# Optimization experiments

Measured on AMD Instinct MI355X. Metric: run time of the kernel, lower is better.

Reference implementation:

```python
import jax, jax.numpy as jnp
import numpy as np

N, D, M, H, FF, L = 8192, 14, 36, 256, 2048, 2  # rows, d_model, material feats, mlp hidden, ffn, layers
EPS = 1e-5


def _ln(x, g, b):
    mu = jnp.mean(x, axis=-1, keepdims=True)
    var = jnp.mean((x - mu) ** 2, axis=-1, keepdims=True)
    return (x - mu) * jax.lax.rsqrt(var + EPS) * g + b


def setup_inputs() -> dict:
    key = jax.random.key(0)
    ks = iter(jax.random.split(key, 32))
    p = lambda shape, fan: jax.random.normal(next(ks), shape, jnp.float32) * (fan ** -0.5)
    return {
        "x": jax.random.normal(next(ks), (N, D), jnp.float32),
        "y": jax.random.normal(next(ks), (N, M), jnp.float32),
        # 2 post-LN TransformerEncoderLayers (nhead=1, dim_feedforward=2048, relu)
        "attn_wqkv": p((L, 3 * D, D), D), "attn_bqkv": p((L, 3 * D), D),
        "attn_wo": p((L, D, D), D), "attn_bo": p((L, D), D),
        "ln1_g": jnp.ones((L, D)), "ln1_b": jnp.zeros((L, D)),
        "ff_w1": p((L, FF, D), D), "ff_b1": p((L, FF), D),
        "ff_w2": p((L, D, FF), FF), "ff_b2": p((L, D), FF),
        "ln2_g": jnp.ones((L, D)), "ln2_b": jnp.zeros((L, D)),
        "fc1_w": p((D, D), D), "fc1_b": p((D,), D),
        "fc2_w": p((1, D), D), "fc2_b": p((1,), D),
        "fc3_w": p((H, D + M + 1), D + M + 1), "fc3_b": p((H,), D + M + 1),
        "fc4_w": p((H, H), H), "fc4_b": p((H,), H),
        "fc5_w": p((1, H), H), "fc5_b": p((1,), H),
    }


def reference(x, y, attn_wqkv, attn_bqkv, attn_wo, attn_bo, ln1_g, ln1_b,
              ff_w1, ff_b1, ff_w2, ff_b2, ln2_g, ln2_b,
              fc1_w, fc1_b, fc2_w, fc2_b, fc3_w, fc3_b, fc4_w, fc4_b, fc5_w, fc5_b):
    h = x  # [N, D]; batch of size 1 squeezed away
    for l in range(L):
        qkv = h @ attn_wqkv[l].T + attn_bqkv[l]            # [N, 3D]
        q, k, v = jnp.split(qkv, 3, axis=-1)
        scores = (q @ k.T) * (D ** -0.5)                   # [N, N]
        a = jax.nn.softmax(scores, axis=-1) @ v            # [N, D]
        a = a @ attn_wo[l].T + attn_bo[l]
        h = _ln(h + a, ln1_g[l], ln1_b[l])
        f = jax.nn.relu(h @ ff_w1[l].T + ff_b1[l]) @ ff_w2[l].T + ff_b2[l]
        h = _ln(h + f, ln2_g[l], ln2_b[l])
    x1 = h @ fc1_w.T + fc1_b                               # [N, D]
    size_out = (x1 @ fc2_w.T + fc2_b)[:, 0]                # [N]

    # batched replacement of the per-row python loop
    size_int = size_out.astype(jnp.int32)                  # trunc toward zero, like .int()
    size_f = size_int.astype(jnp.float32)[:, None]         # [N, 1]
    reg_in = jnp.concatenate([size_f, x, y], axis=1)       # [N, 1+D+M]
    r = jax.nn.relu(reg_in @ fc3_w.T + fc3_b)
    r = jax.nn.relu(r @ fc4_w.T + fc4_b)
    reg_values = (r @ fc5_w.T + fc5_b)[:, 0]               # [N]
    reg_values = jnp.where(size_int != 0, reg_values, 0.0)
    return size_out, reg_values
```

## Files before the change

### kernel.cpp

```cpp
#include <hip/hip_runtime.h>
#include <math.h>

#define NN 8192
#define DD 14
#define DP 16
#define FF 2048
#define HID 256
#define LN_EPS 1e-5f
#define QSCALE (1.4426950408889634f / 3.7416573867739413f)

typedef short bf16x8 __attribute__((ext_vector_type(8)));
typedef float f32x4 __attribute__((ext_vector_type(4)));

#define LOAD16(dst, srcp) { \
  const float4* _p = (const float4*)(srcp); \
  float4 _a = _p[0], _b = _p[1], _c = _p[2], _d = _p[3]; \
  dst[0]=_a.x; dst[1]=_a.y; dst[2]=_a.z; dst[3]=_a.w; \
  dst[4]=_b.x; dst[5]=_b.y; dst[6]=_b.z; dst[7]=_b.w; \
  dst[8]=_c.x; dst[9]=_c.y; dst[10]=_c.z; dst[11]=_c.w; \
  dst[12]=_d.x; dst[13]=_d.y; dst[14]=_d.z; dst[15]=_d.w; }

#define STORE16(dstp, src) { \
  float4* _p = (float4*)(dstp); \
  _p[0] = make_float4(src[0], src[1], src[2], src[3]); \
  _p[1] = make_float4(src[4], src[5], src[6], src[7]); \
  _p[2] = make_float4(src[8], src[9], src[10], src[11]); \
  _p[3] = make_float4(src[12], src[13], src[14], src[15]); }

static __device__ __forceinline__ float fast_exp2(float x) {
#if __has_builtin(__builtin_amdgcn_exp2f)
  return __builtin_amdgcn_exp2f(x);
#else
  return exp2f(x);
#endif
}

static __device__ __forceinline__ unsigned short bf_hi(float x) {
  return (unsigned short)(__float_as_uint(x) >> 16);
}
static __device__ __forceinline__ float bf_hi_f(float x) {
  return __uint_as_float(__float_as_uint(x) & 0xffff0000u);
}

static __device__ __forceinline__ void split8(const float* pv, bf16x8* ph, bf16x8* pl) {
  #pragma unroll
  for (int i = 0; i < 8; i++) {
    unsigned int u = __float_as_uint(pv[i]);
    (*ph)[i] = (short)(u >> 16);
    float rr = pv[i] - __uint_as_float(u & 0xffff0000u);
    (*pl)[i] = (short)(__float_as_uint(rr) >> 16);
  }
}

static __device__ __forceinline__ void qkv_compute_store(
    int r, const float* hr, const float* __restrict__ wqkv,
    const float* __restrict__ bqkv, unsigned int* __restrict__ Qpack,
    unsigned int* __restrict__ KB1, unsigned int* __restrict__ KB2,
    unsigned short* __restrict__ VhiT, unsigned short* __restrict__ VloT) {
  float q[14], k[14], v[14];
  #pragma unroll 6
  for (int c = 0; c < 42; c++) {
    const float* w = wqkv + c * 14;
    float s = bqkv[c];
    #pragma unroll
    for (int d = 0; d < 14; d++) s = fmaf(hr[d], w[d], s);
    if (c < 14)       q[c] = s * QSCALE;
    else if (c < 28)  k[c - 14] = s;
    else              v[c - 28] = s;
  }
  unsigned int qp[16], k1[16], k2[16];
  unsigned short qh[14], ql[14], kh[14], kl[14];
  #pragma unroll
  for (int d = 0; d < 14; d++) {
    qh[d] = bf_hi(q[d]);
    ql[d] = bf_hi(q[d] - bf_hi_f(q[d]));
    kh[d] = bf_hi(k[d]);
    kl[d] = bf_hi(k[d] - bf_hi_f(k[d]));
  }
  #pragma unroll
  for (int i = 0; i < 7; i++) {
    qp[i]     = (unsigned int)qh[2*i] | ((unsigned int)qh[2*i+1] << 16);
    qp[8 + i] = (unsigned int)ql[2*i] | ((unsigned int)ql[2*i+1] << 16);
    k1[i]     = (unsigned int)kh[2*i] | ((unsigned int)kh[2*i+1] << 16);
    k1[8 + i] = k1[i];
    k2[i]     = (unsigned int)kl[2*i] | ((unsigned int)kl[2*i+1] << 16);
    k2[8 + i] = k2[i];
  }
  qp[7] = 0; qp[15] = 0; k1[7] = 0; k1[15] = 0; k2[7] = 0; k2[15] = 0;
  uint4* Qp4 = (uint4*)(Qpack + (size_t)r * 16);
  uint4* K14 = (uint4*)(KB1 + (size_t)r * 16);
  uint4* K24 = (uint4*)(KB2 + (size_t)r * 16);
  #pragma unroll
  for (int i = 0; i < 4; i++) {
    Qp4[i] = make_uint4(qp[4*i], qp[4*i+1], qp[4*i+2], qp[4*i+3]);
    K14[i] = make_uint4(k1[4*i], k1[4*i+1], k1[4*i+2], k1[4*i+3]);
    K24[i] = make_uint4(k2[4*i], k2[4*i+1], k2[4*i+2], k2[4*i+3]);
  }
  #pragma unroll
  for (int d = 0; d < 14; d++) {
    VhiT[(size_t)d * NN + r] = bf_hi(v[d]);
    VloT[(size_t)d * NN + r] = bf_hi(v[d] - bf_hi_f(v[d]));
  }
  VhiT[(size_t)14 * NN + r] = 0x3F80;
  VhiT[(size_t)15 * NN + r] = 0;
  VloT[(size_t)14 * NN + r] = 0;
  VloT[(size_t)15 * NN + r] = 0;
}

static __device__ __forceinline__ void store_apack(unsigned int* dst, const float* o) {
  unsigned int qp[16];
  unsigned short hh[14], ll[14];
  #pragma unroll
  for (int d = 0; d < 14; d++) {
    hh[d] = bf_hi(o[d]);
    ll[d] = bf_hi(o[d] - bf_hi_f(o[d]));
  }
  #pragma unroll
  for (int i = 0; i < 7; i++) {
    qp[i]     = (unsigned int)hh[2*i] | ((unsigned int)hh[2*i+1] << 16);
    qp[8 + i] = (unsigned int)ll[2*i] | ((unsigned int)ll[2*i+1] << 16);
  }
  qp[7] = 0; qp[15] = 0;
  uint4* d4 = (uint4*)dst;
  #pragma unroll
  for (int i = 0; i < 4; i++)
    d4[i] = make_uint4(qp[4*i], qp[4*i+1], qp[4*i+2], qp[4*i+3]);
}

__global__ void pack_all(const float* __restrict__ w3, const float* __restrict__ w4,
                         const float* __restrict__ ffw1, const float* __restrict__ ffw2,
                         const float* __restrict__ x, const float* __restrict__ wqkv,
                         const float* __restrict__ bqkv, float* __restrict__ h,
                         unsigned int* __restrict__ Qpack,
                         unsigned int* __restrict__ KB1, unsigned int* __restrict__ KB2,
                         unsigned short* __restrict__ VhiT, unsigned short* __restrict__ VloT,
                         unsigned short* __restrict__ B3h, unsigned short* __restrict__ B3l,
                         unsigned short* __restrict__ B4h, unsigned short* __restrict__ B4l,
                         unsigned int* __restrict__ W1B1, unsigned int* __restrict__ W1B2,
                         unsigned short* __restrict__ W2h, unsigned short* __restrict__ W2l) {
  const int blk = blockIdx.x, tid = threadIdx.x;
  if (blk < 32) {
    int t = blk * 256 + tid;
    int lane = t & 63, ks = (t >> 6) & 7, nt = t >> 9;
    int n = nt * 16 + (lane & 15);
    int k0 = ks * 32 + (lane >> 4) * 8;
    unsigned int h4[4], l4[4];
    #pragma unroll
    for (int jj = 0; jj < 4; jj++) {
      unsigned short h2[2], l2[2];
      #pragma unroll
      for (int e = 0; e < 2; e++) {
        float v = w4[(size_t)n * 256 + k0 + jj * 2 + e];
        h2[e] = bf_hi(v);
        l2[e] = bf_hi(v - bf_hi_f(v));
      }
      h4[jj] = (unsigned int)h2[0] | ((unsigned int)h2[1] << 16);
      l4[jj] = (unsigned int)l2[0] | ((unsigned int)l2[1] << 16);
    }
    ((uint4*)B4h)[t] = make_uint4(h4[0], h4[1], h4[2], h4[3]);
    ((uint4*)B4l)[t] = make_uint4(l4[0], l4[1], l4[2], l4[3]);
    if (ks < 2) {
      int fi = (nt * 2 + ks) * 64 + lane;
      #pragma unroll
      for (int jj = 0; jj < 4; jj++) {
        unsigned short h2[2], l2[2];
        #pragma unroll
        for (int e = 0; e < 2; e++) {
          int k = k0 + jj * 2 + e;
          float v = (k < 51) ? w3[(size_t)n * 51 + k] : 0.f;
          h2[e] = bf_hi(v);
          l2[e] = bf_hi(v - bf_hi_f(v));
        }
        h4[jj] = (unsigned int)h2[0] | ((unsigned int)h2[1] << 16);
        l4[jj] = (unsigned int)l2[0] | ((unsigned int)l2[1] << 16);
      }
      ((uint4*)B3h)[fi] = make_uint4(h4[0], h4[1], h4[2], h4[3]);
      ((uint4*)B3l)[fi] = make_uint4(l4[0], l4[1], l4[2], l4[3]);
    }
  } else if (blk < 48) {
    int t = (blk - 32) * 256 + tid;
    int l = t >> 11, j = t & 2047;
    const float* wrow = ffw1 + ((size_t)l * FF + j) * 14;
    unsigned int k1[16], k2[16];
    unsigned short kh[14], kl[14];
    #pragma unroll
    for (int d = 0; d < 14; d++) {
      float v = wrow[d];
      kh[d] = bf_hi(v);
      kl[d] = bf_hi(v - bf_hi_f(v));
    }
    #pragma unroll
    for (int i = 0; i < 7; i++) {
      k1[i] = (unsigned int)kh[2*i] | ((unsigned int)kh[2*i+1] << 16);
      k1[8 + i] = k1[i];
      k2[i] = (unsigned int)kl[2*i] | ((unsigned int)kl[2*i+1] << 16);
      k2[8 + i] = k2[i];
    }
    k1[7] = 0; k1[15] = 0; k2[7] = 0; k2[15] = 0;
    uint4* d1 = (uint4*)(W1B1 + (size_t)t * 16);
    uint4* d2 = (uint4*)(W1B2 + (size_t)t * 16);
    #pragma unroll
    for (int i = 0; i < 4; i++) {
      d1[i] = make_uint4(k1[4*i], k1[4*i+1], k1[4*i+2], k1[4*i+3]);
      d2[i] = make_uint4(k2[4*i], k2[4*i+1], k2[4*i+2], k2[4*i+3]);
    }
  } else if (blk < 64) {
    int t = (blk - 48) * 256 + tid;
    int l = t >> 11, j = t & 2047;
    #pragma unroll
    for (int d = 0; d < 16; d++) {
      float v = (d < 14) ? ffw2[((size_t)l * 14 + d) * FF + j] : 0.f;
      W2h[((size_t)l * 16 + d) * FF + j] = bf_hi(v);
      W2l[((size_t)l * 16 + d) * FF + j] = bf_hi(v - bf_hi_f(v));
    }
  } else {
    int r = (blk - 64) * 256 + tid;
    float hr[16];
    #pragma unroll
    for (int d = 0; d < 14; d++) hr[d] = x[(size_t)r * 14 + d];
    hr[14] = 0.f; hr[15] = 0.f;
    STORE16(h + (size_t)r * DP, hr);
    qkv_compute_store(r, hr, wqkv, bqkv, Qpack, KB1, KB2, VhiT, VloT);
  }
}

__global__ __launch_bounds__(512, 2) void attn_flash(
    const unsigned int* __restrict__ Qpack, const unsigned int* __restrict__ KB1,
    const unsigned int* __restrict__ KB2, const unsigned short* __restrict__ VhiT,
    const unsigned short* __restrict__ VloT, float* __restrict__ h,
    const float* __restrict__ wo, const float* __restrict__ bo,
    const float* __restrict__ g, const float* __restrict__ b,
    unsigned int* __restrict__ Hpack) {
  __shared__ float Plds[8][32][36];
  __shared__ float sacc[8][32][16];
  const int tid = threadIdx.x;
  const int wave = tid >> 6;
  const int lane = tid & 63;
  const int lo4 = lane & 15;
  const int hi4 = lane >> 4;
  const int qbase = blockIdx.x * 32;

  const bf16x8* Qp = (const bf16x8*)Qpack;
  const bf16x8* B1 = (const bf16x8*)KB1;
  const bf16x8* B2 = (const bf16x8*)KB2;
  const bf16x8* Vh = (const bf16x8*)VhiT;
  const bf16x8* Vl = (const bf16x8*)VloT;

  bf16x8 aQ0 = Qp[(size_t)(qbase + lo4) * 4 + hi4];
  bf16x8 aQ1 = Qp[(size_t)(qbase + 16 + lo4) * 4 + hi4];
  f32x4 acc0 = {0.f, 0.f, 0.f, 0.f};
  f32x4 acc1 = {0.f, 0.f, 0.f, 0.f};
  const f32x4 zero = {0.f, 0.f, 0.f, 0.f};

  const int kstart = wave * 1024;
  for (int c = 0; c < 32; c++) {
    const int kb = kstart + c * 32;
    bf16x8 b1g0 = B1[(size_t)(kb + lo4) * 4 + hi4];
    bf16x8 b2g0 = B2[(size_t)(kb + lo4) * 4 + hi4];
    bf16x8 b1g1 = B1[(size_t)(kb + 16 + lo4) * 4 + hi4];
    bf16x8 b2g1 = B2[(size_t)(kb + 16 + lo4) * 4 + hi4];
    bf16x8 vh = Vh[(size_t)lo4 * 1024 + (kb >> 3) + hi4];
    bf16x8 vl = Vl[(size_t)lo4 * 1024 + (kb >> 3) + hi4];

    f32x4 s00 = __builtin_amdgcn_mfma_f32_16x16x32_bf16(aQ0, b1g0, zero, 0, 0, 0);
    f32x4 s01 = __builtin_amdgcn_mfma_f32_16x16x32_bf16(aQ0, b1g1, zero, 0, 0, 0);
    f32x4 s10 = __builtin_amdgcn_mfma_f32_16x16x32_bf16(aQ1, b1g0, zero, 0, 0, 0);
    f32x4 s11 = __builtin_amdgcn_mfma_f32_16x16x32_bf16(aQ1, b1g1, zero, 0, 0, 0);
    s00 = __builtin_amdgcn_mfma_f32_16x16x32_bf16(aQ0, b2g0, s00, 0, 0, 0);
    s01 = __builtin_amdgcn_mfma_f32_16x16x32_bf16(aQ0, b2g1, s01, 0, 0, 0);
    s10 = __builtin_amdgcn_mfma_f32_16x16x32_bf16(aQ1, b2g0, s10, 0, 0, 0);
    s11 = __builtin_amdgcn_mfma_f32_16x16x32_bf16(aQ1, b2g1, s11, 0, 0, 0);
    #pragma unroll
    for (int reg = 0; reg < 4; reg++) {
      Plds[wave][hi4 * 4 + reg][lo4]           = fast_exp2(s00[reg]);
      Plds[wave][hi4 * 4 + reg][16 + lo4]      = fast_exp2(s01[reg]);
      Plds[wave][16 + hi4 * 4 + reg][lo4]      = fast_exp2(s10[reg]);
      Plds[wave][16 + hi4 * 4 + reg][16 + lo4] = fast_exp2(s11[reg]);
    }
    __asm__ volatile("s_waitcnt lgkmcnt(0)" ::: "memory");
    const float4* p0 = (const float4*)&Plds[wave][lo4][hi4 * 8];
    const float4* p1 = (const float4*)&Plds[wave][16 + lo4][hi4 * 8];
    float4 a0 = p0[0], a1 = p0[1], c0 = p1[0], c1 = p1[1];
    float pv0[8] = {a0.x, a0.y, a0.z, a0.w, a1.x, a1.y, a1.z, a1.w};
    float pv1[8] = {c0.x, c0.y, c0.z, c0.w, c1.x, c1.y, c1.z, c1.w};
    bf16x8 ph0, pl0, ph1, pl1;
    split8(pv0, &ph0, &pl0);
    split8(pv1, &ph1, &pl1);
    acc0 = __builtin_amdgcn_mfma_f32_16x16x32_bf16(ph0, vh, acc0, 0, 0, 0);
    acc1 = __builtin_amdgcn_mfma_f32_16x16x32_bf16(ph1, vh, acc1, 0, 0, 0);
    acc0 = __builtin_amdgcn_mfma_f32_16x16x32_bf16(pl0, vh, acc0, 0, 0, 0);
    acc1 = __builtin_amdgcn_mfma_f32_16x16x32_bf16(pl1, vh, acc1, 0, 0, 0);
    acc0 = __builtin_amdgcn_mfma_f32_16x16x32_bf16(ph0, vl, acc0, 0, 0, 0);
    acc1 = __builtin_amdgcn_mfma_f32_16x16x32_bf16(ph1, vl, acc1, 0, 0, 0);
    __asm__ volatile("s_waitcnt lgkmcnt(0)" ::: "memory");
  }

  #pragma unroll
  for (int reg = 0; reg < 4; reg++) {
    sacc[wave][hi4 * 4 + reg][lo4] = acc0[reg];
    sacc[wave][16 + hi4 * 4 + reg][lo4] = acc1[reg];
  }
  __syncthreads();
  {
    int qq = tid >> 4, col = tid & 15;
    float v = 0.f;
    #pragma unroll
    for (int w = 0; w < 8; w++) v += sacc[w][qq][col];
    sacc[0][qq][col] = v;
  }
  __syncthreads();

  if (tid < 32) {
    int r = qbase + tid;
    float L = sacc[0][tid][14];
    float inv = 1.f / L;
    float a[14];
    #pragma unroll
    for (int d = 0; d < 14; d++) a[d] = sacc[0][tid][d] * inv;
    float hr[16];
    LOAD16(hr, h + (size_t)r * DP);
    float xx[14];
    #pragma unroll
    for (int i = 0; i < 14; i++) {
      float s = bo[i];
      #pragma unroll
      for (int d = 0; d < 14; d++) s = fmaf(wo[i * 14 + d], a[d], s);
      xx[i] = hr[i] + s;
    }
    float mu = 0.f;
    #pragma unroll
    for (int i = 0; i < 14; i++) mu += xx[i];
    mu *= (1.f / 14.f);
    float var = 0.f;
    #pragma unroll
    for (int i = 0; i < 14; i++) { float tt = xx[i] - mu; var = fmaf(tt, tt, var); }
    var *= (1.f / 14.f);
    float rs = rsqrtf(var + LN_EPS);
    float o[16];
    #pragma unroll
    for (int i = 0; i < 14; i++) o[i] = fmaf((xx[i] - mu) * rs, g[i], b[i]);
    o[14] = 0.f; o[15] = 0.f;
    STORE16(h + (size_t)r * DP, o);
    store_apack(Hpack + (size_t)r * 16, o);
  }
}

__global__ __launch_bounds__(512, 2) void ffn_flash_qkv(
    float* __restrict__ h, const unsigned int* __restrict__ Hpack,
    const unsigned int* __restrict__ W1B1, const unsigned int* __restrict__ W1B2,
    const unsigned short* __restrict__ W2h, const unsigned short* __restrict__ W2l,
    const float* __restrict__ b1, const float* __restrict__ b2,
    const float* __restrict__ g, const float* __restrict__ bb,
    const float* __restrict__ wqkv, const float* __restrict__ bqkv,
    unsigned int* __restrict__ Qpack, unsigned int* __restrict__ KB1,
    unsigned int* __restrict__ KB2, unsigned short* __restrict__ VhiT,
    unsigned short* __restrict__ VloT) {
  __shared__ float Plds[8][32][36];
  __shared__ float sacc[8][32][16];
  const int tid = threadIdx.x;
  const int wave = tid >> 6;
  const int lane = tid & 63;
  const int lo4 = lane & 15;
  const int hi4 = lane >> 4;
  const int qbase = blockIdx.x * 32;

  const bf16x8* Hp = (const bf16x8*)Hpack;
  const bf16x8* B1 = (const bf16x8*)W1B1;
  const bf16x8* B2 = (const bf16x8*)W1B2;
  const bf16x8* Vh = (const bf16x8*)W2h;
  const bf16x8* Vl = (const bf16x8*)W2l;

  bf16x8 aH0 = Hp[(size_t)(qbase + lo4) * 4 + hi4];
  bf16x8 aH1 = Hp[(size_t)(qbase + 16 + lo4) * 4 + hi4];
  f32x4 acc0 = {0.f, 0.f, 0.f, 0.f};
  f32x4 acc1 = {0.f, 0.f, 0.f, 0.f};
  const f32x4 zero = {0.f, 0.f, 0.f, 0.f};

  const int jstart = wave * 256;
  for (int c = 0; c < 8; c++) {
    const int jb = jstart + c * 32;
    bf16x8 b1g0 = B1[(size_t)(jb + lo4) * 4 + hi4];
    bf16x8 b2g0 = B2[(size_t)(jb + lo4) * 4 + hi4];
    bf16x8 b1g1 = B1[(size_t)(jb + 16 + lo4) * 4 + hi4];
    bf16x8 b2g1 = B2[(size_t)(jb + 16 + lo4) * 4 + hi4];
    bf16x8 vh = Vh[(size_t)lo4 * 256 + (jb >> 3) + hi4];
    bf16x8 vl = Vl[(size_t)lo4 * 256 + (jb >> 3) + hi4];
    float bb0 = b1[jb + lo4];
    float bb1 = b1[jb + 16 + lo4];

    f32x4 s00 = __builtin_amdgcn_mfma_f32_16x16x32_bf16(aH0, b1g0, zero, 0, 0, 0);
    f32x4 s01 = __builtin_amdgcn_mfma_f32_16x16x32_bf16(aH0, b1g1, zero, 0, 0, 0);
    f32x4 s10 = __builtin_amdgcn_mfma_f32_16x16x32_bf16(aH1, b1g0, zero, 0, 0, 0);
    f32x4 s11 = __builtin_amdgcn_mfma_f32_16x16x32_bf16(aH1, b1g1, zero, 0, 0, 0);
    s00 = __builtin_amdgcn_mfma_f32_16x16x32_bf16(aH0, b2g0, s00, 0, 0, 0);
    s01 = __builtin_amdgcn_mfma_f32_16x16x32_bf16(aH0, b2g1, s01, 0, 0, 0);
    s10 = __builtin_amdgcn_mfma_f32_16x16x32_bf16(aH1, b2g0, s10, 0, 0, 0);
    s11 = __builtin_amdgcn_mfma_f32_16x16x32_bf16(aH1, b2g1, s11, 0, 0, 0);
    #pragma unroll
    for (int reg = 0; reg < 4; reg++) {
      Plds[wave][hi4 * 4 + reg][lo4]           = fmaxf(s00[reg] + bb0, 0.f);
      Plds[wave][hi4 * 4 + reg][16 + lo4]      = fmaxf(s01[reg] + bb1, 0.f);
      Plds[wave][16 + hi4 * 4 + reg][lo4]      = fmaxf(s10[reg] + bb0, 0.f);
      Plds[wave][16 + hi4 * 4 + reg][16 + lo4] = fmaxf(s11[reg] + bb1, 0.f);
    }
    __asm__ volatile("s_waitcnt lgkmcnt(0)" ::: "memory");
    const float4* p0 = (const float4*)&Plds[wave][lo4][hi4 * 8];
    const float4* p1 = (const float4*)&Plds[wave][16 + lo4][hi4 * 8];
    float4 a0 = p0[0], a1 = p0[1], c0 = p1[0], c1 = p1[1];
    float pv0[8] = {a0.x, a0.y, a0.z, a0.w, a1.x, a1.y, a1.z, a1.w};
    float pv1[8] = {c0.x, c0.y, c0.z, c0.w, c1.x, c1.y, c1.z, c1.w};
    bf16x8 th0, tl0, th1, tl1;
    split8(pv0, &th0, &tl0);
    split8(pv1, &th1, &tl1);
    acc0 = __builtin_amdgcn_mfma_f32_16x16x32_bf16(th0, vh, acc0, 0, 0, 0);
    acc1 = __builtin_amdgcn_mfma_f32_16x16x32_bf16(th1, vh, acc1, 0, 0, 0);
    acc0 = __builtin_amdgcn_mfma_f32_16x16x32_bf16(tl0, vh, acc0, 0, 0, 0);
    acc1 = __builtin_amdgcn_mfma_f32_16x16x32_bf16(tl1, vh, acc1, 0, 0, 0);
    acc0 = __builtin_amdgcn_mfma_f32_16x16x32_bf16(th0, vl, acc0, 0, 0, 0);
    acc1 = __builtin_amdgcn_mfma_f32_16x16x32_bf16(th1, vl, acc1, 0, 0, 0);
    __asm__ volatile("s_waitcnt lgkmcnt(0)" ::: "memory");
  }

  #pragma unroll
  for (int reg = 0; reg < 4; reg++) {
    sacc[wave][hi4 * 4 + reg][lo4] = acc0[reg];
    sacc[wave][16 + hi4 * 4 + reg][lo4] = acc1[reg];
  }
  __syncthreads();
  {
    int qq = tid >> 4, col = tid & 15;
    float v = 0.f;
    #pragma unroll
    for (int w = 0; w < 8; w++) v += sacc[w][qq][col];
    sacc[0][qq][col] = v;
  }
  __syncthreads();

  if (tid < 32) {
    int r = qbase + tid;
    float hr[16];
    LOAD16(hr, h + (size_t)r * DP);
    float xx[14];
    #pragma unroll
    for (int i = 0; i < 14; i++) xx[i] = hr[i] + sacc[0][tid][i] + b2[i];
    float mu = 0.f;
    #pragma unroll
    for (int i = 0; i < 14; i++) mu += xx[i];
    mu *= (1.f / 14.f);
    float var = 0.f;
    #pragma unroll
    for (int i = 0; i < 14; i++) { float tt = xx[i] - mu; var = fmaf(tt, tt, var); }
    var *= (1.f / 14.f);
    float rs = rsqrtf(var + LN_EPS);
    float o[16];
    #pragma unroll
    for (int i = 0; i < 14; i++) o[i] = fmaf((xx[i] - mu) * rs, g[i], bb[i]);
    o[14] = 0.f; o[15] = 0.f;
    STORE16(h + (size_t)r * DP, o);
    qkv_compute_store(r, o, wqkv, bqkv, Qpack, KB1, KB2, VhiT, VloT);
  }
}

__global__ __launch_bounds__(256, 4) void ffn_tail(
    const float* __restrict__ h, const unsigned int* __restrict__ Hpack,
    const unsigned int* __restrict__ W1B1, const unsigned int* __restrict__ W1B2,
    const unsigned short* __restrict__ W2h, const unsigned short* __restrict__ W2l,
    const float* __restrict__ b1,
    const float* __restrict__ b2, const float* __restrict__ g, const float* __restrict__ b,
    const float* __restrict__ fc1w, const float* __restrict__ fc1b,
    const float* __restrict__ fc2w, const float* __restrict__ fc2b,
    const float* __restrict__ x, const float* __restrict__ y,
    const unsigned short* __restrict__ B3h, const unsigned short* __restrict__ B3l,
    const float* __restrict__ b3,
    const unsigned short* __restrict__ B4h, const unsigned short* __restrict__ B4l,
    const float* __restrict__ b4,
    const float* __restrict__ w5, const float* __restrict__ b5,
    float* __restrict__ out, float* __restrict__ outr) {
  __shared__ float PldsT[4][16][36];
  __shared__ float saccT[4][16][16];
  __shared__ alignas(16) unsigned short Ah[16][72], Al[16][72];
  __shared__ alignas(16) unsigned short R1h[16][264], R1l[16][264];
  __shared__ float sred[4][16][16];
  __shared__ float szf[16];
  const int tid = threadIdx.x;
  const int wave = tid >> 6;
  const int lane = tid & 63;
  const int lo4 = lane & 15;
  const int hi4 = lane >> 4;
  const int rbase = blockIdx.x * 16;
  const f32x4 zero = {0.f, 0.f, 0.f, 0.f};

  {
    const bf16x8* Hp = (const bf16x8*)Hpack;
    const bf16x8* B1 = (const bf16x8*)W1B1;
    const bf16x8* B2 = (const bf16x8*)W1B2;
    const bf16x8* Vh = (const bf16x8*)W2h;
    const bf16x8* Vl = (const bf16x8*)W2l;
    bf16x8 aH0 = Hp[(size_t)(rbase + lo4) * 4 + hi4];
    f32x4 acc0 = zero;
    const int jstart = wave * 512;
    for (int c = 0; c < 16; c++) {
      const int jb = jstart + c * 32;
      bf16x8 b1g0 = B1[(size_t)(jb + lo4) * 4 + hi4];
      bf16x8 b2g0 = B2[(size_t)(jb + lo4) * 4 + hi4];
      bf16x8 b1g1 = B1[(size_t)(jb + 16 + lo4) * 4 + hi4];
      bf16x8 b2g1 = B2[(size_t)(jb + 16 + lo4) * 4 + hi4];
      bf16x8 vh = Vh[(size_t)lo4 * 256 + (jb >> 3) + hi4];
      bf16x8 vl = Vl[(size_t)lo4 * 256 + (jb >> 3) + hi4];
      float bb0 = b1[jb + lo4];
      float bb1 = b1[jb + 16 + lo4];

      f32x4 s00 = __builtin_amdgcn_mfma_f32_16x16x32_bf16(aH0, b1g0, zero, 0, 0, 0);
      f32x4 s01 = __builtin_amdgcn_mfma_f32_16x16x32_bf16(aH0, b1g1, zero, 0, 0, 0);
      s00 = __builtin_amdgcn_mfma_f32_16x16x32_bf16(aH0, b2g0, s00, 0, 0, 0);
      s01 = __builtin_amdgcn_mfma_f32_16x16x32_bf16(aH0, b2g1, s01, 0, 0, 0);
      #pragma unroll
      for (int reg = 0; reg < 4; reg++) {
        PldsT[wave][hi4 * 4 + reg][lo4]      = fmaxf(s00[reg] + bb0, 0.f);
        PldsT[wave][hi4 * 4 + reg][16 + lo4] = fmaxf(s01[reg] + bb1, 0.f);
      }
      __asm__ volatile("s_waitcnt lgkmcnt(0)" ::: "memory");
      const float4* p0 = (const float4*)&PldsT[wave][lo4][hi4 * 8];
      float4 a0 = p0[0], a1 = p0[1];
      float pv0[8] = {a0.x, a0.y, a0.z, a0.w, a1.x, a1.y, a1.z, a1.w};
      bf16x8 th0, tl0;
      split8(pv0, &th0, &tl0);
      acc0 = __builtin_amdgcn_mfma_f32_16x16x32_bf16(th0, vh, acc0, 0, 0, 0);
      acc0 = __builtin_amdgcn_mfma_f32_16x16x32_bf16(tl0, vh, acc0, 0, 0, 0);
      acc0 = __builtin_amdgcn_mfma_f32_16x16x32_bf16(th0, vl, acc0, 0, 0, 0);
      __asm__ volatile("s_waitcnt lgkmcnt(0)" ::: "memory");
    }
    #pragma unroll
    for (int reg = 0; reg < 4; reg++)
      saccT[wave][hi4 * 4 + reg][lo4] = acc0[reg];
  }
  __syncthreads();
  {
    int qq = tid >> 4, col = tid & 15;
    float v = saccT[0][qq][col] + saccT[1][qq][col] + saccT[2][qq][col] + saccT[3][qq][col];
    saccT[0][qq][col] = v;
  }
  __syncthreads();

  if (tid < 16) {
    int r = rbase + tid;
    float hr[16];
    LOAD16(hr, h + (size_t)r * DP);
    float xx[14];
    #pragma unroll
    for (int i = 0; i < 14; i++) xx[i] = hr[i] + saccT[0][tid][i] + b2[i];
    float mu = 0.f;
    #pragma unroll
    for (int i = 0; i < 14; i++) mu += xx[i];
    mu *= (1.f / 14.f);
    float var = 0.f;
    #pragma unroll
    for (int i = 0; i < 14; i++) { float tt = xx[i] - mu; var = fmaf(tt, tt, var); }
    var *= (1.f / 14.f);
    float rs = rsqrtf(var + LN_EPS);
    float o[14];
    #pragma unroll
    for (int i = 0; i < 14; i++) o[i] = fmaf((xx[i] - mu) * rs, g[i], b[i]);
    float s = fc2b[0];
    #pragma unroll
    for (int i = 0; i < 14; i++) {
      float tt = fc1b[i];
      #pragma unroll
      for (int d = 0; d < 14; d++) tt = fmaf(fc1w[i * 14 + d], o[d], tt);
      s = fmaf(tt, fc2w[i], s);
    }
    out[r] = s;
    int si = (int)s;
    szf[tid] = (float)si;
  }
  __syncthreads();

  for (int idx = tid; idx < 16 * 64; idx += 256) {
    int m = idx >> 6, k = idx & 63;
    int r = rbase + m;
    float v = 0.f;
    if (k == 0)       v = szf[m];
    else if (k < 15)  v = x[(size_t)r * 14 + (k - 1)];
    else if (k < 51)  v = y[(size_t)r * 36 + (k - 15)];
    Ah[m][k] = bf_hi(v);
    Al[m][k] = bf_hi(v - bf_hi_f(v));
  }
  __syncthreads();

  f32x4 acc[4];
  #pragma unroll
  for (int nt = 0; nt < 4; nt++) acc[nt] = zero;
  #pragma unroll
  for (int ks = 0; ks < 2; ks++) {
    bf16x8 ah = *(const bf16x8*)&Ah[lo4][ks * 32 + hi4 * 8];
    bf16x8 al = *(const bf16x8*)&Al[lo4][ks * 32 + hi4 * 8];
    #pragma unroll
    for (int nt = 0; nt < 4; nt++) {
      int fi = ((wave * 4 + nt) * 2 + ks) * 64 + lane;
      bf16x8 bh = ((const bf16x8*)B3h)[fi];
      bf16x8 bl = ((const bf16x8*)B3l)[fi];
      acc[nt] = __builtin_amdgcn_mfma_f32_16x16x32_bf16(ah, bh, acc[nt], 0, 0, 0);
      acc[nt] = __builtin_amdgcn_mfma_f32_16x16x32_bf16(al, bh, acc[nt], 0, 0, 0);
      acc[nt] = __builtin_amdgcn_mfma_f32_16x16x32_bf16(ah, bl, acc[nt], 0, 0, 0);
    }
  }
  #pragma unroll
  for (int nt = 0; nt < 4; nt++) {
    int n = (wave * 4 + nt) * 16 + lo4;
    float bbv = b3[n];
    #pragma unroll
    for (int reg = 0; reg < 4; reg++) {
      int m = hi4 * 4 + reg;
      float v = fmaxf(acc[nt][reg] + bbv, 0.f);
      R1h[m][n] = bf_hi(v);
      R1l[m][n] = bf_hi(v - bf_hi_f(v));
    }
  }
  __syncthreads();

  #pragma unroll
  for (int nt = 0; nt < 4; nt++) acc[nt] = zero;
  #pragma unroll
  for (int ks = 0; ks < 8; ks++) {
    bf16x8 ah = *(const bf16x8*)&R1h[lo4][ks * 32 + hi4 * 8];
    bf16x8 al = *(const bf16x8*)&R1l[lo4][ks * 32 + hi4 * 8];
    #pragma unroll
    for (int nt = 0; nt < 4; nt++) {
      int fi = ((wave * 4 + nt) * 8 + ks) * 64 + lane;
      bf16x8 bh = ((const bf16x8*)B4h)[fi];
      bf16x8 bl = ((const bf16x8*)B4l)[fi];
      acc[nt] = __builtin_amdgcn_mfma_f32_16x16x32_bf16(ah, bh, acc[nt], 0, 0, 0);
      acc[nt] = __builtin_amdgcn_mfma_f32_16x16x32_bf16(al, bh, acc[nt], 0, 0, 0);
      acc[nt] = __builtin_amdgcn_mfma_f32_16x16x32_bf16(ah, bl, acc[nt], 0, 0, 0);
    }
  }
  float s4[4] = {0.f, 0.f, 0.f, 0.f};
  #pragma unroll
  for (int nt = 0; nt < 4; nt++) {
    int n = (wave * 4 + nt) * 16 + lo4;
    float bbv = b4[n], ww = w5[n];
    #pragma unroll
    for (int reg = 0; reg < 4; reg++)
      s4[reg] = fmaf(fmaxf(acc[nt][reg] + bbv, 0.f), ww, s4[reg]);
  }
  #pragma unroll
  for (int reg = 0; reg < 4; reg++) sred[wave][hi4 * 4 + reg][lo4] = s4[reg];
  __syncthreads();

  if (tid < 16) {
    float t = b5[0];
    #pragma unroll
    for (int w = 0; w < 4; w++) {
      const float4* p = (const float4*)&sred[w][tid][0];
      float4 a0 = p[0], a1 = p[1], a2 = p[2], a3 = p[3];
      t += ((a0.x + a0.y) + (a0.z + a0.w)) + ((a1.x + a1.y) + (a1.z + a1.w)) +
           ((a2.x + a2.y) + (a2.z + a2.w)) + ((a3.x + a3.y) + (a3.z + a3.w));
    }
    float sz = szf[tid];
    outr[rbase + tid] = (sz != 0.f) ? t : 0.f;
  }
}

extern "C" void kernel_launch(void* const* d_in, const int* in_sizes, int n_in,
                              void* d_out, int out_size, void* d_ws, size_t ws_size,
                              hipStream_t stream) {
  const float* x    = (const float*)d_in[0];
  const float* y    = (const float*)d_in[1];
  const float* wqkv = (const float*)d_in[2];
  const float* bqkv = (const float*)d_in[3];
  const float* wo   = (const float*)d_in[4];
  const float* bo   = (const float*)d_in[5];
  const float* ln1g = (const float*)d_in[6];
  const float* ln1b = (const float*)d_in[7];
  const float* ffw1 = (const float*)d_in[8];
  const float* ffb1 = (const float*)d_in[9];
  const float* ffw2 = (const float*)d_in[10];
  const float* ffb2 = (const float*)d_in[11];
  const float* ln2g = (const float*)d_in[12];
  const float* ln2b = (const float*)d_in[13];
  const float* fc1w = (const float*)d_in[14];
  const float* fc1b = (const float*)d_in[15];
  const float* fc2w = (const float*)d_in[16];
  const float* fc2b = (const float*)d_in[17];
  const float* fc3w = (const float*)d_in[18];
  const float* fc3b = (const float*)d_in[19];
  const float* fc4w = (const float*)d_in[20];
  const float* fc4b = (const float*)d_in[21];
  const float* fc5w = (const float*)d_in[22];
  const float* fc5b = (const float*)d_in[23];

  float* ws = (float*)d_ws;
  float*          h     = ws;
  unsigned int*   Qpack = (unsigned int*)(ws + 131072);
  unsigned int*   KB1   = (unsigned int*)(ws + 262144);
  unsigned int*   KB2   = (unsigned int*)(ws + 393216);
  unsigned short* VhiT  = (unsigned short*)(ws + 524288);
  unsigned short* VloT  = (unsigned short*)(ws + 589824);
  unsigned int*   Hpack = (unsigned int*)(ws + 655360);
  unsigned short* B3h   = (unsigned short*)(ws + 2891776);
  unsigned short* B3l   = (unsigned short*)(ws + 2899968);
  unsigned short* B4h   = (unsigned short*)(ws + 2908160);
  unsigned short* B4l   = (unsigned short*)(ws + 2940928);
  unsigned int*   W1B1  = (unsigned int*)(ws + 2973696);
  unsigned int*   W1B2  = (unsigned int*)(ws + 3039232);
  unsigned short* W2h   = (unsigned short*)(ws + 3104768);
  unsigned short* W2l   = (unsigned short*)(ws + 3137536);

  float* out = (float*)d_out;

  pack_all<<<96, 256, 0, stream>>>(fc3w, fc4w, ffw1, ffw2, x, wqkv, bqkv, h,
                                   Qpack, KB1, KB2, VhiT, VloT,
                                   B3h, B3l, B4h, B4l, W1B1, W1B2, W2h, W2l);

  attn_flash<<<256, 512, 0, stream>>>(Qpack, KB1, KB2, VhiT, VloT, h,
                                      wo, bo, ln1g, ln1b, Hpack);
  ffn_flash_qkv<<<256, 512, 0, stream>>>(h, Hpack, W1B1, W1B2, W2h, W2l,
                                         ffb1, ffb2, ln2g, ln2b,
                                         wqkv + 42 * 14, bqkv + 42,
                                         Qpack, KB1, KB2, VhiT, VloT);
  attn_flash<<<256, 512, 0, stream>>>(Qpack, KB1, KB2, VhiT, VloT, h,
                                      wo + 196, bo + 14, ln1g + 14, ln1b + 14, Hpack);
  ffn_tail<<<512, 256, 0, stream>>>(h, Hpack,
                                    W1B1 + (size_t)2048 * 16, W1B2 + (size_t)2048 * 16,
                                    W2h + (size_t)16 * FF, W2l + (size_t)16 * FF,
                                    ffb1 + FF, ffb2 + 14, ln2g + 14, ln2b + 14,
                                    fc1w, fc1b, fc2w, fc2b, x, y,
                                    B3h, B3l, fc3b, B4h, B4l, fc4b,
                                    fc5w, fc5b, out, out + NN);
}
```

Baseline: 244.9 us.

## Fuse attention with FFN per layer and software-pipeline the P·V stage

Merges each layer's attention and FFN kernels into one kernel, so five launches become three and the intermediate h/Hpack round trip through global memory goes away. Layer-1 QKV now goes into separate double buffers, so the fused layer-0 kernel never overwrites inputs that other blocks are still reading. Both the attention and FFN inner loops are software-pipelined: the LDS read and P·V MFMA for chunk c-1 are issued after the score MFMAs for chunk c, which drops the explicit lgkmcnt waits. The tail MLP now handles 32 rows per 512-thread block. The costs are more shared memory, higher register pressure, and an occupancy hint of 4 blocks per CU that may not be reachable.

```diff
diff --git a/kernel.cpp b/kernel.cpp
--- a/kernel.cpp
+++ b/kernel.cpp
@@ -125,6 +125,37 @@
   #pragma unroll
   for (int i = 0; i < 4; i++)
     d4[i] = make_uint4(qp[4*i], qp[4*i+1], qp[4*i+2], qp[4*i+3]);
+}
+
+static __device__ __forceinline__ void combine_ln1(
+    const float* srow, const float* hr, const float* __restrict__ wo,
+    const float* __restrict__ bo, const float* __restrict__ g,
+    const float* __restrict__ b, float* o) {
+  float L = srow[14];
+  float inv = 1.f / L;
+  float a[14];
+  #pragma unroll
+  for (int d = 0; d < 14; d++) a[d] = srow[d] * inv;
+  float xx[14];
+  #pragma unroll
+  for (int i = 0; i < 14; i++) {
+    float s = bo[i];
+    #pragma unroll
+    for (int d = 0; d < 14; d++) s = fmaf(wo[i * 14 + d], a[d], s);
+    xx[i] = hr[i] + s;
+  }
+  float mu = 0.f;
+  #pragma unroll
+  for (int i = 0; i < 14; i++) mu += xx[i];
+  mu *= (1.f / 14.f);
+  float var = 0.f;
+  #pragma unroll
+  for (int i = 0; i < 14; i++) { float tt = xx[i] - mu; var = fmaf(tt, tt, var); }
+  var *= (1.f / 14.f);
+  float rs = rsqrtf(var + LN_EPS);
+  #pragma unroll
+  for (int i = 0; i < 14; i++) o[i] = fmaf((xx[i] - mu) * rs, g[i], b[i]);
+  o[14] = 0.f; o[15] = 0.f;
 }
 
 __global__ void pack_all(const float* __restrict__ w3, const float* __restrict__ w4,
@@ -224,37 +255,26 @@
   }
 }
 
-__global__ __launch_bounds__(512, 2) void attn_flash(
-    const unsigned int* __restrict__ Qpack, const unsigned int* __restrict__ KB1,
-    const unsigned int* __restrict__ KB2, const unsigned short* __restrict__ VhiT,
-    const unsigned short* __restrict__ VloT, float* __restrict__ h,
-    const float* __restrict__ wo, const float* __restrict__ bo,
-    const float* __restrict__ g, const float* __restrict__ b,
-    unsigned int* __restrict__ Hpack) {
-  __shared__ float Plds[8][32][36];
-  __shared__ float sacc[8][32][16];
-  const int tid = threadIdx.x;
-  const int wave = tid >> 6;
-  const int lane = tid & 63;
-  const int lo4 = lane & 15;
-  const int hi4 = lane >> 4;
-  const int qbase = blockIdx.x * 32;
-
-  const bf16x8* Qp = (const bf16x8*)Qpack;
-  const bf16x8* B1 = (const bf16x8*)KB1;
-  const bf16x8* B2 = (const bf16x8*)KB2;
-  const bf16x8* Vh = (const bf16x8*)VhiT;
-  const bf16x8* Vl = (const bf16x8*)VloT;
-
+static __device__ __forceinline__ void attn_core(
+    const bf16x8* __restrict__ Qp, const bf16x8* __restrict__ B1,
+    const bf16x8* __restrict__ B2, const bf16x8* __restrict__ Vh,
+    const bf16x8* __restrict__ Vl, int qbase, int wave, int lo4, int hi4,
+    float (*Pl)[36], f32x4* o0, f32x4* o1) {
+  const f32x4 zero = {0.f, 0.f, 0.f, 0.f};
   bf16x8 aQ0 = Qp[(size_t)(qbase + lo4) * 4 + hi4];
   bf16x8 aQ1 = Qp[(size_t)(qbase + 16 + lo4) * 4 + hi4];
-  f32x4 acc0 = {0.f, 0.f, 0.f, 0.f};
-  f32x4 acc1 = {0.f, 0.f, 0.f, 0.f};
-  const f32x4 zero = {0.f, 0.f, 0.f, 0.f};
-
+  f32x4 acc0 = zero, acc1 = zero;
   const int kstart = wave * 1024;
+  float4 ra0, ra1, rc0, rc1;
+  const float4* p0 = (const float4*)&Pl[lo4][hi4 * 8];
+  const float4* p1 = (const float4*)&Pl[16 + lo4][hi4 * 8];
+
   for (int c = 0; c < 32; c++) {
     const int kb = kstart + c * 32;
+    if (c > 0) {
+      ra0 = p0[0]; ra1 = p0[1]; rc0 = p1[0]; rc1 = p1[1];
+      __asm__ volatile("" ::: "memory");
+    }
     bf16x8 b1g0 = B1[(size_t)(kb + lo4) * 4 + hi4];
     bf16x8 b2g0 = B2[(size_t)(kb + lo4) * 4 + hi4];
     bf16x8 b1g1 = B1[(size_t)(kb + 16 + lo4) * 4 + hi4];
@@ -272,119 +292,69 @@
     s11 = __builtin_amdgcn_mfma_f32_16x16x32_bf16(aQ1, b2g1, s11, 0, 0, 0);
     #pragma unroll
     for (int reg = 0; reg < 4; reg++) {
-      Plds[wave][hi4 * 4 + reg][lo4]           = fast_exp2(s00[reg]);
-      Plds[wave][hi4 * 4 + reg][16 + lo4]      = fast_exp2(s01[reg]);
-      Plds[wave][16 + hi4 * 4 + reg][lo4]      = fast_exp2(s10[reg]);
-      Plds[wave][16 + hi4 * 4 + reg][16 + lo4] = fast_exp2(s11[reg]);
-    }
-    __asm__ volatile("s_waitcnt lgkmcnt(0)" ::: "memory");
-    const float4* p0 = (const float4*)&Plds[wave][lo4][hi4 * 8];
-    const float4* p1 = (const float4*)&Plds[wave][16 + lo4][hi4 * 8];
+      Pl[hi4 * 4 + reg][lo4]           = fast_exp2(s00[reg]);
+      Pl[hi4 * 4 + reg][16 + lo4]      = fast_exp2(s01[reg]);
+      Pl[16 + hi4 * 4 + reg][lo4]      = fast_exp2(s10[reg]);
+      Pl[16 + hi4 * 4 + reg][16 + lo4] = fast_exp2(s11[reg]);
+    }
+    if (c > 0) {
+      const int kbp = kb - 32;
+      bf16x8 vhp = Vh[(size_t)lo4 * 1024 + (kbp >> 3) + hi4];
+      bf16x8 vlp = Vl[(size_t)lo4 * 1024 + (kbp >> 3) + hi4];
+      float pv0[8] = {ra0.x, ra0.y, ra0.z, ra0.w, ra1.x, ra1.y, ra1.z, ra1.w};
+      float pv1[8] = {rc0.x, rc0.y, rc0.z, rc0.w, rc1.x, rc1.y, rc1.z, rc1.w};
+      bf16x8 ph0, pl0, ph1, pl1;
+      split8(pv0, &ph0, &pl0);
+      split8(pv1, &ph1, &pl1);
+      acc0 = __builtin_amdgcn_mfma_f32_16x16x32_bf16(ph0, vhp, acc0, 0, 0, 0);
+      acc1 = __builtin_amdgcn_mfma_f32_16x16x32_bf16(ph1, vhp, acc1, 0, 0, 0);
+      acc0 = __builtin_amdgcn_mfma_f32_16x16x32_bf16(pl0, vhp, acc0, 0, 0, 0);
+      acc1 = __builtin_amdgcn_mfma_f32_16x16x32_bf16(pl1, vhp, acc1, 0, 0, 0);
+      acc0 = __builtin_amdgcn_mfma_f32_16x16x32_bf16(ph0, vlp, acc0, 0, 0, 0);
+      acc1 = __builtin_amdgcn_mfma_f32_16x16x32_bf16(ph1, vlp, acc1, 0, 0, 0);
+    }
+  }
+  {
+    const int kbp = kstart + 31 * 32;
+    bf16x8 vhp = Vh[(size_t)lo4 * 1024 + (kbp >> 3) + hi4];
+    bf16x8 vlp = Vl[(size_t)lo4 * 1024 + (kbp >> 3) + hi4];
     float4 a0 = p0[0], a1 = p0[1], c0 = p1[0], c1 = p1[1];
     float pv0[8] = {a0.x, a0.y, a0.z, a0.w, a1.x, a1.y, a1.z, a1.w};
     float pv1[8] = {c0.x, c0.y, c0.z, c0.w, c1.x, c1.y, c1.z, c1.w};
     bf16x8 ph0, pl0, ph1, pl1;
     split8(pv0, &ph0, &pl0);
     split8(pv1, &ph1, &pl1);
-    acc0 = __builtin_amdgcn_mfma_f32_16x16x32_bf16(ph0, vh, acc0, 0, 0, 0);
-    acc1 = __builtin_amdgcn_mfma_f32_16x16x32_bf16(ph1, vh, acc1, 0, 0, 0);
-    acc0 = __builtin_amdgcn_mfma_f32_16x16x32_bf16(pl0, vh, acc0, 0, 0, 0);
-    acc1 = __builtin_amdgcn_mfma_f32_16x16x32_bf16(pl1, vh, acc1, 0, 0, 0);
-    acc0 = __builtin_amdgcn_mfma_f32_16x16x32_bf16(ph0, vl, acc0, 0, 0, 0);
-    acc1 = __builtin_amdgcn_mfma_f32_16x16x32_bf16(ph1, vl, acc1, 0, 0, 0);
-    __asm__ volatile("s_waitcnt lgkmcnt(0)" ::: "memory");
-  }
-
-  #pragma unroll
-  for (int reg = 0; reg < 4; reg++) {
-    sacc[wave][hi4 * 4 + reg][lo4] = acc0[reg];
-    sacc[wave][16 + hi4 * 4 + reg][lo4] = acc1[reg];
-  }
-  __syncthreads();
-  {
-    int qq = tid >> 4, col = tid & 15;
-    float v = 0.f;
-    #pragma unroll
-    for (int w = 0; w < 8; w++) v += sacc[w][qq][col];
-    sacc[0][qq][col] = v;
-  }
-  __syncthreads();
-
-  if (tid < 32) {
-    int r = qbase + tid;
-    float L = sacc[0][tid][14];
-    float inv = 1.f / L;
-    float a[14];
-    #pragma unroll
-    for (int d = 0; d < 14; d++) a[d] = sacc[0][tid][d] * inv;
-    float hr[16];
-    LOAD16(hr, h + (size_t)r * DP);
-    float xx[14];
-    #pragma unroll
-    for (int i = 0; i < 14; i++) {
-      float s = bo[i];
-      #pragma unroll
-      for (int d = 0; d < 14; d++) s = fmaf(wo[i * 14 + d], a[d], s);
-      xx[i] = hr[i] + s;
-    }
-    float mu = 0.f;
-    #pragma unroll
-    for (int i = 0; i < 14; i++) mu += xx[i];
-    mu *= (1.f / 14.f);
-    float var = 0.f;
-    #pragma unroll
-    for (int i = 0; i < 14; i++) { float tt = xx[i] - mu; var = fmaf(tt, tt, var); }
-    var *= (1.f / 14.f);
-    float rs = rsqrtf(var + LN_EPS);
-    float o[16];
-    #pragma unroll
-    for (int i = 0; i < 14; i++) o[i] = fmaf((xx[i] - mu) * rs, g[i], b[i]);
-    o[14] = 0.f; o[15] = 0.f;
-    STORE16(h + (size_t)r * DP, o);
-    store_apack(Hpack + (size_t)r * 16, o);
-  }
-}
-
-__global__ __launch_bounds__(512, 2) void ffn_flash_qkv(
-    float* __restrict__ h, const unsigned int* __restrict__ Hpack,
-    const unsigned int* __restrict__ W1B1, const unsigned int* __restrict__ W1B2,
-    const unsigned short* __restrict__ W2h, const unsigned short* __restrict__ W2l,
-    const float* __restrict__ b1, const float* __restrict__ b2,
-    const float* __restrict__ g, const float* __restrict__ bb,
-    const float* __restrict__ wqkv, const float* __restrict__ bqkv,
-    unsigned int* __restrict__ Qpack, unsigned int* __restrict__ KB1,
-    unsigned int* __restrict__ KB2, unsigned short* __restrict__ VhiT,
-    unsigned short* __restrict__ VloT) {
-  __shared__ float Plds[8][32][36];
-  __shared__ float sacc[8][32][16];
-  const int tid = threadIdx.x;
-  const int wave = tid >> 6;
-  const int lane = tid & 63;
-  const int lo4 = lane & 15;
-  const int hi4 = lane >> 4;
-  const int qbase = blockIdx.x * 32;
-
-  const bf16x8* Hp = (const bf16x8*)Hpack;
-  const bf16x8* B1 = (const bf16x8*)W1B1;
-  const bf16x8* B2 = (const bf16x8*)W1B2;
-  const bf16x8* Vh = (const bf16x8*)W2h;
-  const bf16x8* Vl = (const bf16x8*)W2l;
-
-  bf16x8 aH0 = Hp[(size_t)(qbase + lo4) * 4 + hi4];
-  bf16x8 aH1 = Hp[(size_t)(qbase + 16 + lo4) * 4 + hi4];
-  f32x4 acc0 = {0.f, 0.f, 0.f, 0.f};
-  f32x4 acc1 = {0.f, 0.f, 0.f, 0.f};
+    acc0 = __builtin_amdgcn_mfma_f32_16x16x32_bf16(ph0, vhp, acc0, 0, 0, 0);
+    acc1 = __builtin_amdgcn_mfma_f32_16x16x32_bf16(ph1, vhp, acc1, 0, 0, 0);
+    acc0 = __builtin_amdgcn_mfma_f32_16x16x32_bf16(pl0, vhp, acc0, 0, 0, 0);
+    acc1 = __builtin_amdgcn_mfma_f32_16x16x32_bf16(pl1, vhp, acc1, 0, 0, 0);
+    acc0 = __builtin_amdgcn_mfma_f32_16x16x32_bf16(ph0, vlp, acc0, 0, 0, 0);
+    acc1 = __builtin_amdgcn_mfma_f32_16x16x32_bf16(ph1, vlp, acc1, 0, 0, 0);
+  }
+  *o0 = acc0; *o1 = acc1;
+}
+
+static __device__ __forceinline__ void ffn_core(
+    bf16x8 aH0, bf16x8 aH1, const bf16x8* __restrict__ B1,
+    const bf16x8* __restrict__ B2, const bf16x8* __restrict__ Vh,
+    const bf16x8* __restrict__ Vl, const float* __restrict__ b1,
+    int jstart, int lo4, int hi4, float (*Pl)[36], f32x4* o0, f32x4* o1) {
   const f32x4 zero = {0.f, 0.f, 0.f, 0.f};
-
-  const int jstart = wave * 256;
+  f32x4 acc0 = zero, acc1 = zero;
+  float4 ra0, ra1, rc0, rc1;
+  const float4* p0 = (const float4*)&Pl[lo4][hi4 * 8];
+  const float4* p1 = (const float4*)&Pl[16 + lo4][hi4 * 8];
+
   for (int c = 0; c < 8; c++) {
     const int jb = jstart + c * 32;
+    if (c > 0) {
+      ra0 = p0[0]; ra1 = p0[1]; rc0 = p1[0]; rc1 = p1[1];
+      __asm__ volatile("" ::: "memory");
+    }
     bf16x8 b1g0 = B1[(size_t)(jb + lo4) * 4 + hi4];
     bf16x8 b2g0 = B2[(size_t)(jb + lo4) * 4 + hi4];
     bf16x8 b1g1 = B1[(size_t)(jb + 16 + lo4) * 4 + hi4];
     bf16x8 b2g1 = B2[(size_t)(jb + 16 + lo4) * 4 + hi4];
-    bf16x8 vh = Vh[(size_t)lo4 * 256 + (jb >> 3) + hi4];
-    bf16x8 vl = Vl[(size_t)lo4 * 256 + (jb >> 3) + hi4];
     float bb0 = b1[jb + lo4];
     float bb1 = b1[jb + 16 + lo4];
 
@@ -398,33 +368,85 @@
     s11 = __builtin_amdgcn_mfma_f32_16x16x32_bf16(aH1, b2g1, s11, 0, 0, 0);
     #pragma unroll
     for (int reg = 0; reg < 4; reg++) {
-      Plds[wave][hi4 * 4 + reg][lo4]           = fmaxf(s00[reg] + bb0, 0.f);
-      Plds[wave][hi4 * 4 + reg][16 + lo4]      = fmaxf(s01[reg] + bb1, 0.f);
-      Plds[wave][16 + hi4 * 4 + reg][lo4]      = fmaxf(s10[reg] + bb0, 0.f);
-      Plds[wave][16 + hi4 * 4 + reg][16 + lo4] = fmaxf(s11[reg] + bb1, 0.f);
-    }
-    __asm__ volatile("s_waitcnt lgkmcnt(0)" ::: "memory");
-    const float4* p0 = (const float4*)&Plds[wave][lo4][hi4 * 8];
-    const float4* p1 = (const float4*)&Plds[wave][16 + lo4][hi4 * 8];
+      Pl[hi4 * 4 + reg][lo4]           = fmaxf(s00[reg] + bb0, 0.f);
+      Pl[hi4 * 4 + reg][16 + lo4]      = fmaxf(s01[reg] + bb1, 0.f);
+      Pl[16 + hi4 * 4 + reg][lo4]      = fmaxf(s10[reg] + bb0, 0.f);
+      Pl[16 + hi4 * 4 + reg][16 + lo4] = fmaxf(s11[reg] + bb1, 0.f);
+    }
+    if (c > 0) {
+      const int jbp = jb - 32;
+      bf16x8 vhp = Vh[(size_t)lo4 * 256 + (jbp >> 3) + hi4];
+      bf16x8 vlp = Vl[(size_t)lo4 * 256 + (jbp >> 3) + hi4];
+      float pv0[8] = {ra0.x, ra0.y, ra0.z, ra0.w, ra1.x, ra1.y, ra1.z, ra1.w};
+      float pv1[8] = {rc0.x, rc0.y, rc0.z, rc0.w, rc1.x, rc1.y, rc1.z, rc1.w};
+      bf16x8 th0, tl0, th1, tl1;
+      split8(pv0, &th0, &tl0);
+      split8(pv1, &th1, &tl1);
+      acc0 = __builtin_amdgcn_mfma_f32_16x16x32_bf16(th0, vhp, acc0, 0, 0, 0);
+      acc1 = __builtin_amdgcn_mfma_f32_16x16x32_bf16(th1, vhp, acc1, 0, 0, 0);
+      acc0 = __builtin_amdgcn_mfma_f32_16x16x32_bf16(tl0, vhp, acc0, 0, 0, 0);
+      acc1 = __builtin_amdgcn_mfma_f32_16x16x32_bf16(tl1, vhp, acc1, 0, 0, 0);
+      acc0 = __builtin_amdgcn_mfma_f32_16x16x32_bf16(th0, vlp, acc0, 0, 0, 0);
+      acc1 = __builtin_amdgcn_mfma_f32_16x16x32_bf16(th1, vlp, acc1, 0, 0, 0);
+    }
+  }
+  {
+    const int jbp = jstart + 7 * 32;
+    bf16x8 vhp = Vh[(size_t)lo4 * 256 + (jbp >> 3) + hi4];
+    bf16x8 vlp = Vl[(size_t)lo4 * 256 + (jbp >> 3) + hi4];
     float4 a0 = p0[0], a1 = p0[1], c0 = p1[0], c1 = p1[1];
     float pv0[8] = {a0.x, a0.y, a0.z, a0.w, a1.x, a1.y, a1.z, a1.w};
     float pv1[8] = {c0.x, c0.y, c0.z, c0.w, c1.x, c1.y, c1.z, c1.w};
     bf16x8 th0, tl0, th1, tl1;
     split8(pv0, &th0, &tl0);
     split8(pv1, &th1, &tl1);
-    acc0 = __builtin_amdgcn_mfma_f32_16x16x32_bf16(th0, vh, acc0, 0, 0, 0);
-    acc1 = __builtin_amdgcn_mfma_f32_16x16x32_bf16(th1, vh, acc1, 0, 0, 0);
-    acc0 = __builtin_amdgcn_mfma_f32_16x16x32_bf16(tl0, vh, acc0, 0, 0, 0);
-    acc1 = __builtin_amdgcn_mfma_f32_16x16x32_bf16(tl1, vh, acc1, 0, 0, 0);
-    acc0 = __builtin_amdgcn_mfma_f32_16x16x32_bf16(th0, vl, acc0, 0, 0, 0);
-    acc1 = __builtin_amdgcn_mfma_f32_16x16x32_bf16(th1, vl, acc1, 0, 0, 0);
-    __asm__ volatile("s_waitcnt lgkmcnt(0)" ::: "memory");
-  }
-
+    acc0 = __builtin_amdgcn_mfma_f32_16x16x32_bf16(th0, vhp, acc0, 0, 0, 0);
+    acc1 = __builtin_amdgcn_mfma_f32_16x16x32_bf16(th1, vhp, acc1, 0, 0, 0);
+    acc0 = __builtin_amdgcn_mfma_f32_16x16x32_bf16(tl0, vhp, acc0, 0, 0, 0);
+    acc1 = __builtin_amdgcn_mfma_f32_16x16x32_bf16(tl1, vhp, acc1, 0, 0, 0);
+    acc0 = __builtin_amdgcn_mfma_f32_16x16x32_bf16(th0, vlp, acc0, 0, 0, 0);
+    acc1 = __builtin_amdgcn_mfma_f32_16x16x32_bf16(th1, vlp, acc1, 0, 0, 0);
+  }
+  *o0 = acc0; *o1 = acc1;
+}
+
+#define SMEM_BYTES 57472
+
+__global__ __launch_bounds__(512, 4) void layer0_fused(
+    const unsigned int* __restrict__ Qpack, const unsigned int* __restrict__ KB1,
+    const unsigned int* __restrict__ KB2, const unsigned short* __restrict__ VhiT,
+    const unsigned short* __restrict__ VloT, float* __restrict__ h,
+    const float* __restrict__ wo, const float* __restrict__ bo,
+    const float* __restrict__ g1, const float* __restrict__ b1n,
+    const unsigned int* __restrict__ W1B1, const unsigned int* __restrict__ W1B2,
+    const unsigned short* __restrict__ W2h, const unsigned short* __restrict__ W2l,
+    const float* __restrict__ fb1, const float* __restrict__ fb2,
+    const float* __restrict__ g2, const float* __restrict__ b2n,
+    const float* __restrict__ wqkv1, const float* __restrict__ bqkv1,
+    unsigned int* __restrict__ Qpack1, unsigned int* __restrict__ KB1_1,
+    unsigned int* __restrict__ KB2_1, unsigned short* __restrict__ VhiT1,
+    unsigned short* __restrict__ VloT1) {
+  __shared__ alignas(16) char smem[SMEM_BYTES];
+  const int tid = threadIdx.x;
+  const int wave = tid >> 6;
+  const int lane = tid & 63;
+  const int lo4 = lane & 15;
+  const int hi4 = lane >> 4;
+  const int qbase = blockIdx.x * 32;
+
+  float (*Pl)[36] = (float(*)[36])(smem + wave * 4608);
+  float (*sacc)[32][16] = (float(*)[32][16])(smem + 36864);
+  float (*hrow)[16] = (float(*)[16])(smem + 53248);
+  unsigned int (*Hl)[16] = (unsigned int(*)[16])(smem + 55296);
+
+  f32x4 a0, a1;
+  attn_core((const bf16x8*)Qpack, (const bf16x8*)KB1, (const bf16x8*)KB2,
+            (const bf16x8*)VhiT, (const bf16x8*)VloT, qbase, wave, lo4, hi4,
+            Pl, &a0, &a1);
   #pragma unroll
   for (int reg = 0; reg < 4; reg++) {
-    sacc[wave][hi4 * 4 + reg][lo4] = acc0[reg];
-    sacc[wave][16 + hi4 * 4 + reg][lo4] = acc1[reg];
+    sacc[wave][hi4 * 4 + reg][lo4] = a0[reg];
+    sacc[wave][16 + hi4 * 4 + reg][lo4] = a1[reg];
   }
   __syncthreads();
   {
@@ -435,14 +457,44 @@
     sacc[0][qq][col] = v;
   }
   __syncthreads();
-
   if (tid < 32) {
     int r = qbase + tid;
     float hr[16];
     LOAD16(hr, h + (size_t)r * DP);
+    float o[16];
+    combine_ln1(&sacc[0][tid][0], hr, wo, bo, g1, b1n, o);
+    #pragma unroll
+    for (int i = 0; i < 16; i++) hrow[tid][i] = o[i];
+    store_apack(&Hl[tid][0], o);
+  }
+  __syncthreads();
+
+  bf16x8 aH0 = *(const bf16x8*)&Hl[lo4][hi4 * 4];
+  bf16x8 aH1 = *(const bf16x8*)&Hl[16 + lo4][hi4 * 4];
+  f32x4 f0, f1;
+  ffn_core(aH0, aH1, (const bf16x8*)W1B1, (const bf16x8*)W1B2,
+           (const bf16x8*)W2h, (const bf16x8*)W2l, fb1, wave * 256,
+           lo4, hi4, Pl, &f0, &f1);
+  __syncthreads();
+  #pragma unroll
+  for (int reg = 0; reg < 4; reg++) {
+    sacc[wave][hi4 * 4 + reg][lo4] = f0[reg];
+    sacc[wave][16 + hi4 * 4 + reg][lo4] = f1[reg];
+  }
+  __syncthreads();
+  {
+    int qq = tid >> 4, col = tid & 15;
+    float v = 0.f;
+    #pragma unroll
+    for (int w = 0; w < 8; w++) v += sacc[w][qq][col];
+    sacc[0][qq][col] = v;
+  }
+  __syncthreads();
+  if (tid < 32) {
+    int r = qbase + tid;
     float xx[14];
     #pragma unroll
-    for (int i = 0; i < 14; i++) xx[i] = hr[i] + sacc[0][tid][i] + b2[i];
+    for (int i = 0; i < 14; i++) xx[i] = hrow[tid][i] + sacc[0][tid][i] + fb2[i];
     float mu = 0.f;
     #pragma unroll
     for (int i = 0; i < 14; i++) mu += xx[i];
@@ -454,19 +506,23 @@
     float rs = rsqrtf(var + LN_EPS);
     float o[16];
     #pragma unroll
-    for (int i = 0; i < 14; i++) o[i] = fmaf((xx[i] - mu) * rs, g[i], bb[i]);
+    for (int i = 0; i < 14; i++) o[i] = fmaf((xx[i] - mu) * rs, g2[i], b2n[i]);
     o[14] = 0.f; o[15] = 0.f;
     STORE16(h + (size_t)r * DP, o);
-    qkv_compute_store(r, o, wqkv, bqkv, Qpack, KB1, KB2, VhiT, VloT);
-  }
-}
-
-__global__ __launch_bounds__(256, 4) void ffn_tail(
-    const float* __restrict__ h, const unsigned int* __restrict__ Hpack,
+    qkv_compute_store(r, o, wqkv1, bqkv1, Qpack1, KB1_1, KB2_1, VhiT1, VloT1);
+  }
+}
+
+__global__ __launch_bounds__(512, 4) void layer1_tail(
+    const unsigned int* __restrict__ Qpack, const unsigned int* __restrict__ KB1,
+    const unsigned int* __restrict__ KB2, const unsigned short* __restrict__ VhiT,
+    const unsigned short* __restrict__ VloT, const float* __restrict__ h,
+    const float* __restrict__ wo, const float* __restrict__ bo,
+    const float* __restrict__ g1, const float* __restrict__ b1n,
     const unsigned int* __restrict__ W1B1, const unsigned int* __restrict__ W1B2,
     const unsigned short* __restrict__ W2h, const unsigned short* __restrict__ W2l,
-    const float* __restrict__ b1,
-    const float* __restrict__ b2, const float* __restrict__ g, const float* __restrict__ b,
+    const float* __restrict__ fb1, const float* __restrict__ fb2,
+    const float* __restrict__ g2, const float* __restrict__ b2n,
     const float* __restrict__ fc1w, const float* __restrict__ fc1b,
     const float* __restrict__ fc2w, const float* __restrict__ fc2b,
     const float* __restrict__ x, const float* __restrict__ y,
@@ -476,79 +532,77 @@
     const float* __restrict__ b4,
     const float* __restrict__ w5, const float* __restrict__ b5,
     float* __restrict__ out, float* __restrict__ outr) {
-  __shared__ float PldsT[4][16][36];
-  __shared__ float saccT[4][16][16];
-  __shared__ alignas(16) unsigned short Ah[16][72], Al[16][72];
-  __shared__ alignas(16) unsigned short R1h[16][264], R1l[16][264];
-  __shared__ float sred[4][16][16];
-  __shared__ float szf[16];
+  __shared__ alignas(16) char smem[SMEM_BYTES];
   const int tid = threadIdx.x;
   const int wave = tid >> 6;
   const int lane = tid & 63;
   const int lo4 = lane & 15;
   const int hi4 = lane >> 4;
-  const int rbase = blockIdx.x * 16;
+  const int qbase = blockIdx.x * 32;
   const f32x4 zero = {0.f, 0.f, 0.f, 0.f};
 
-  {
-    const bf16x8* Hp = (const bf16x8*)Hpack;
-    const bf16x8* B1 = (const bf16x8*)W1B1;
-    const bf16x8* B2 = (const bf16x8*)W1B2;
-    const bf16x8* Vh = (const bf16x8*)W2h;
-    const bf16x8* Vl = (const bf16x8*)W2l;
-    bf16x8 aH0 = Hp[(size_t)(rbase + lo4) * 4 + hi4];
-    f32x4 acc0 = zero;
-    const int jstart = wave * 512;
-    for (int c = 0; c < 16; c++) {
-      const int jb = jstart + c * 32;
-      bf16x8 b1g0 = B1[(size_t)(jb + lo4) * 4 + hi4];
-      bf16x8 b2g0 = B2[(size_t)(jb + lo4) * 4 + hi4];
-      bf16x8 b1g1 = B1[(size_t)(jb + 16 + lo4) * 4 + hi4];
-      bf16x8 b2g1 = B2[(size_t)(jb + 16 + lo4) * 4 + hi4];
-      bf16x8 vh = Vh[(size_t)lo4 * 256 + (jb >> 3) + hi4];
-      bf16x8 vl = Vl[(size_t)lo4 * 256 + (jb >> 3) + hi4];
-      float bb0 = b1[jb + lo4];
-      float bb1 = b1[jb + 16 + lo4];
-
-      f32x4 s00 = __builtin_amdgcn_mfma_f32_16x16x32_bf16(aH0, b1g0, zero, 0, 0, 0);
-      f32x4 s01 = __builtin_amdgcn_mfma_f32_16x16x32_bf16(aH0, b1g1, zero, 0, 0, 0);
-      s00 = __builtin_amdgcn_mfma_f32_16x16x32_bf16(aH0, b2g0, s00, 0, 0, 0);
-      s01 = __builtin_amdgcn_mfma_f32_16x16x32_bf16(aH0, b2g1, s01, 0, 0, 0);
-      #pragma unroll
-      for (int reg = 0; reg < 4; reg++) {
-        PldsT[wave][hi4 * 4 + reg][lo4]      = fmaxf(s00[reg] + bb0, 0.f);
-        PldsT[wave][hi4 * 4 + reg][16 + lo4] = fmaxf(s01[reg] + bb1, 0.f);
-      }
-      __asm__ volatile("s_waitcnt lgkmcnt(0)" ::: "memory");
-      const float4* p0 = (const float4*)&PldsT[wave][lo4][hi4 * 8];
-      float4 a0 = p0[0], a1 = p0[1];
-      float pv0[8] = {a0.x, a0.y, a0.z, a0.w, a1.x, a1.y, a1.z, a1.w};
-      bf16x8 th0, tl0;
-      split8(pv0, &th0, &tl0);
-      acc0 = __builtin_amdgcn_mfma_f32_16x16x32_bf16(th0, vh, acc0, 0, 0, 0);
-      acc0 = __builtin_amdgcn_mfma_f32_16x16x32_bf16(tl0, vh, acc0, 0, 0, 0);
-      acc0 = __builtin_amdgcn_mfma_f32_16x16x32_bf16(th0, vl, acc0, 0, 0, 0);
-      __asm__ volatile("s_waitcnt lgkmcnt(0)" ::: "memory");
-    }
-    #pragma unroll
-    for (int reg = 0; reg < 4; reg++)
-      saccT[wave][hi4 * 4 + reg][lo4] = acc0[reg];
+  float (*Pl)[36] = (float(*)[36])(smem + wave * 4608);
+  float (*sacc)[32][16] = (float(*)[32][16])(smem + 36864);
+  float (*hrow)[16] = (float(*)[16])(smem + 53248);
+  unsigned int (*Hl)[16] = (unsigned int(*)[16])(smem + 55296);
+  float* szf = (float*)(smem + 57344);
+
+  f32x4 a0, a1;
+  attn_core((const bf16x8*)Qpack, (const bf16x8*)KB1, (const bf16x8*)KB2,
+            (const bf16x8*)VhiT, (const bf16x8*)VloT, qbase, wave, lo4, hi4,
+            Pl, &a0, &a1);
+  #pragma unroll
+  for (int reg = 0; reg < 4; reg++) {
+    sacc[wave][hi4 * 4 + reg][lo4] = a0[reg];
+    sacc[wave][16 + hi4 * 4 + reg][lo4] = a1[reg];
   }
   __syncthreads();
   {
     int qq = tid >> 4, col = tid & 15;
-    float v = saccT[0][qq][col] + saccT[1][qq][col] + saccT[2][qq][col] + saccT[3][qq][col];
-    saccT[0][qq][col] = v;
-  }
-  __syncthreads();
-
-  if (tid < 16) {
-    int r = rbase + tid;
+    float v = 0.f;
+    #pragma unroll
+    for (int w = 0; w < 8; w++) v += sacc[w][qq][col];
+    sacc[0][qq][col] = v;
+  }
+  __syncthreads();
+  if (tid < 32) {
+    int r = qbase + tid;
     float hr[16];
     LOAD16(hr, h + (size_t)r * DP);
+    float o[16];
+    combine_ln1(&sacc[0][tid][0], hr, wo, bo, g1, b1n, o);
+    #pragma unroll
+    for (int i = 0; i < 16; i++) hrow[tid][i] = o[i];
+    store_apack(&Hl[tid][0], o);
+  }
+  __syncthreads();
+
+  bf16x8 aH0 = *(const bf16x8*)&Hl[lo4][hi4 * 4];
+  bf16x8 aH1 = *(const bf16x8*)&Hl[16 + lo4][hi4 * 4];
+  f32x4 f0, f1;
+  ffn_core(aH0, aH1, (const bf16x8*)W1B1, (const bf16x8*)W1B2,
+           (const bf16x8*)W2h, (const bf16x8*)W2l, fb1, wave * 256,
+           lo4, hi4, Pl, &f0, &f1);
+  __syncthreads();
+  #pragma unroll
+  for (int reg = 0; reg < 4; reg++) {
+    sacc[wave][hi4 * 4 + reg][lo4] = f0[reg];
+    sacc[wave][16 + hi4 * 4 + reg][lo4] = f1[reg];
+  }
+  __syncthreads();
+  {
+    int qq = tid >> 4, col = tid & 15;
+    float v = 0.f;
+    #pragma unroll
+    for (int w = 0; w < 8; w++) v += sacc[w][qq][col];
+    sacc[0][qq][col] = v;
+  }
+  __syncthreads();
+  if (tid < 32) {
+    int r = qbase + tid;
     float xx[14];
     #pragma unroll
-    for (int i = 0; i < 14; i++) xx[i] = hr[i] + saccT[0][tid][i] + b2[i];
+    for (int i = 0; i < 14; i++) xx[i] = hrow[tid][i] + sacc[0][tid][i] + fb2[i];
     float mu = 0.f;
     #pragma unroll
     for (int i = 0; i < 14; i++) mu += xx[i];
@@ -560,7 +614,7 @@
     float rs = rsqrtf(var + LN_EPS);
     float o[14];
     #pragma unroll
-    for (int i = 0; i < 14; i++) o[i] = fmaf((xx[i] - mu) * rs, g[i], b[i]);
+    for (int i = 0; i < 14; i++) o[i] = fmaf((xx[i] - mu) * rs, g2[i], b2n[i]);
     float s = fc2b[0];
     #pragma unroll
     for (int i = 0; i < 14; i++) {
@@ -575,17 +629,26 @@
   }
   __syncthreads();
 
-  for (int idx = tid; idx < 16 * 64; idx += 256) {
-    int m = idx >> 6, k = idx & 63;
-    int r = rbase + m;
+  const int grp = wave >> 2;
+  const int wg  = wave & 3;
+
+  for (int idx = tid; idx < 2 * 16 * 64; idx += 512) {
+    int g = idx >> 10, m = (idx >> 6) & 15, k = idx & 63;
+    int r = qbase + g * 16 + m;
     float v = 0.f;
-    if (k == 0)       v = szf[m];
+    if (k == 0)       v = szf[g * 16 + m];
     else if (k < 15)  v = x[(size_t)r * 14 + (k - 1)];
     else if (k < 51)  v = y[(size_t)r * 36 + (k - 15)];
-    Ah[m][k] = bf_hi(v);
-    Al[m][k] = bf_hi(v - bf_hi_f(v));
-  }
-  __syncthreads();
+    ((unsigned short(*)[72])(smem + g * 2304))[m][k] = bf_hi(v);
+    ((unsigned short(*)[72])(smem + 4608 + g * 2304))[m][k] = bf_hi(v - bf_hi_f(v));
+  }
+  __syncthreads();
+
+  unsigned short (*Ah)[72]  = (unsigned short(*)[72])(smem + grp * 2304);
+  unsigned short (*Al)[72]  = (unsigned short(*)[72])(smem + 4608 + grp * 2304);
+  unsigned short (*R1h)[264] = (unsigned short(*)[264])(smem + 9216 + grp * 8448);
+  unsigned short (*R1l)[264] = (unsigned short(*)[264])(smem + 26112 + grp * 8448);
+  float (*sred)[16][16] = (float(*)[16][16])(smem + 43008 + (size_t)grp * 4096);
 
   f32x4 acc[4];
   #pragma unroll
@@ -596,7 +659,7 @@
     bf16x8 al = *(const bf16x8*)&Al[lo4][ks * 32 + hi4 * 8];
     #pragma unroll
     for (int nt = 0; nt < 4; nt++) {
-      int fi = ((wave * 4 + nt) * 2 + ks) * 64 + lane;
+      int fi = ((wg * 4 + nt) * 2 + ks) * 64 + lane;
       bf16x8 bh = ((const bf16x8*)B3h)[fi];
       bf16x8 bl = ((const bf16x8*)B3l)[fi];
       acc[nt] = __builtin_amdgcn_mfma_f32_16x16x32_bf16(ah, bh, acc[nt], 0, 0, 0);
@@ -606,7 +669,7 @@
   }
   #pragma unroll
   for (int nt = 0; nt < 4; nt++) {
-    int n = (wave * 4 + nt) * 16 + lo4;
+    int n = (wg * 4 + nt) * 16 + lo4;
     float bbv = b3[n];
     #pragma unroll
     for (int reg = 0; reg < 4; reg++) {
@@ -626,7 +689,7 @@
     bf16x8 al = *(const bf16x8*)&R1l[lo4][ks * 32 + hi4 * 8];
     #pragma unroll
     for (int nt = 0; nt < 4; nt++) {
-      int fi = ((wave * 4 + nt) * 8 + ks) * 64 + lane;
+      int fi = ((wg * 4 + nt) * 8 + ks) * 64 + lane;
       bf16x8 bh = ((const bf16x8*)B4h)[fi];
       bf16x8 bl = ((const bf16x8*)B4l)[fi];
       acc[nt] = __builtin_amdgcn_mfma_f32_16x16x32_bf16(ah, bh, acc[nt], 0, 0, 0);
@@ -637,27 +700,29 @@
   float s4[4] = {0.f, 0.f, 0.f, 0.f};
   #pragma unroll
   for (int nt = 0; nt < 4; nt++) {
-    int n = (wave * 4 + nt) * 16 + lo4;
+    int n = (wg * 4 + nt) * 16 + lo4;
     float bbv = b4[n], ww = w5[n];
     #pragma unroll
     for (int reg = 0; reg < 4; reg++)
       s4[reg] = fmaf(fmaxf(acc[nt][reg] + bbv, 0.f), ww, s4[reg]);
   }
   #pragma unroll
-  for (int reg = 0; reg < 4; reg++) sred[wave][hi4 * 4 + reg][lo4] = s4[reg];
-  __syncthreads();
-
-  if (tid < 16) {
+  for (int reg = 0; reg < 4; reg++) sred[wg][hi4 * 4 + reg][lo4] = s4[reg];
+  __syncthreads();
+
+  if (tid < 32) {
+    int g = tid >> 4, m = tid & 15;
+    float (*sredG)[16][16] = (float(*)[16][16])(smem + 43008 + (size_t)g * 4096);
     float t = b5[0];
     #pragma unroll
     for (int w = 0; w < 4; w++) {
-      const float4* p = (const float4*)&sred[w][tid][0];
-      float4 a0 = p[0], a1 = p[1], a2 = p[2], a3 = p[3];
-      t += ((a0.x + a0.y) + (a0.z + a0.w)) + ((a1.x + a1.y) + (a1.z + a1.w)) +
-           ((a2.x + a2.y) + (a2.z + a2.w)) + ((a3.x + a3.y) + (a3.z + a3.w));
+      const float4* p = (const float4*)&sredG[w][m][0];
+      float4 q0 = p[0], q1 = p[1], q2 = p[2], q3 = p[3];
+      t += ((q0.x + q0.y) + (q0.z + q0.w)) + ((q1.x + q1.y) + (q1.z + q1.w)) +
+           ((q2.x + q2.y) + (q2.z + q2.w)) + ((q3.x + q3.y) + (q3.z + q3.w));
     }
     float sz = szf[tid];
-    outr[rbase + tid] = (sz != 0.f) ? t : 0.f;
+    outr[qbase + tid] = (sz != 0.f) ? t : 0.f;
   }
 }
 
@@ -690,41 +755,46 @@
   const float* fc5b = (const float*)d_in[23];
 
   float* ws = (float*)d_ws;
-  float*          h     = ws;
-  unsigned int*   Qpack = (unsigned int*)(ws + 131072);
-  unsigned int*   KB1   = (unsigned int*)(ws + 262144);
-  unsigned int*   KB2   = (unsigned int*)(ws + 393216);
-  unsigned short* VhiT  = (unsigned short*)(ws + 524288);
-  unsigned short* VloT  = (unsigned short*)(ws + 589824);
-  unsigned int*   Hpack = (unsigned int*)(ws + 655360);
-  unsigned short* B3h   = (unsigned short*)(ws + 2891776);
-  unsigned short* B3l   = (unsigned short*)(ws + 2899968);
-  unsigned short* B4h   = (unsigned short*)(ws + 2908160);
-  unsigned short* B4l   = (unsigned short*)(ws + 2940928);
-  unsigned int*   W1B1  = (unsigned int*)(ws + 2973696);
-  unsigned int*   W1B2  = (unsigned int*)(ws + 3039232);
-  unsigned short* W2h   = (unsigned short*)(ws + 3104768);
-  unsigned short* W2l   = (unsigned short*)(ws + 3137536);
+  float*          h      = ws;
+  unsigned int*   Qpack0 = (unsigned int*)(ws + 131072);
+  unsigned int*   KB1_0  = (unsigned int*)(ws + 262144);
+  unsigned int*   KB2_0  = (unsigned int*)(ws + 393216);
+  unsigned short* VhiT0  = (unsigned short*)(ws + 524288);
+  unsigned short* VloT0  = (unsigned short*)(ws + 589824);
+  unsigned int*   Qpack1 = (unsigned int*)(ws + 786432);
+  unsigned int*   KB1_1  = (unsigned int*)(ws + 917504);
+  unsigned int*   KB2_1  = (unsigned int*)(ws + 1048576);
+  unsigned short* VhiT1  = (unsigned short*)(ws + 1179648);
+  unsigned short* VloT1  = (unsigned short*)(ws + 1245184);
+  unsigned short* B3h    = (unsigned short*)(ws + 2891776);
+  unsigned short* B3l    = (unsigned short*)(ws + 2899968);
+  unsigned short* B4h    = (unsigned short*)(ws + 2908160);
+  unsigned short* B4l    = (unsigned short*)(ws + 2940928);
+  unsigned int*   W1B1   = (unsigned int*)(ws + 2973696);
+  unsigned int*   W1B2   = (unsigned int*)(ws + 3039232);
+  unsigned short* W2h    = (unsigned short*)(ws + 3104768);
+  unsigned short* W2l    = (unsigned short*)(ws + 3137536);
 
   float* out = (float*)d_out;
 
   pack_all<<<96, 256, 0, stream>>>(fc3w, fc4w, ffw1, ffw2, x, wqkv, bqkv, h,
-                                   Qpack, KB1, KB2, VhiT, VloT,
+                                   Qpack0, KB1_0, KB2_0, VhiT0, VloT0,
                                    B3h, B3l, B4h, B4l, W1B1, W1B2, W2h, W2l);
 
-  attn_flash<<<256, 512, 0, stream>>>(Qpack, KB1, KB2, VhiT, VloT, h,
-                                      wo, bo, ln1g, ln1b, Hpack);
-  ffn_flash_qkv<<<256, 512, 0, stream>>>(h, Hpack, W1B1, W1B2, W2h, W2l,
-                                         ffb1, ffb2, ln2g, ln2b,
-                                         wqkv + 42 * 14, bqkv + 42,
-                                         Qpack, KB1, KB2, VhiT, VloT);
-  attn_flash<<<256, 512, 0, stream>>>(Qpack, KB1, KB2, VhiT, VloT, h,
-                                      wo + 196, bo + 14, ln1g + 14, ln1b + 14, Hpack);
-  ffn_tail<<<512, 256, 0, stream>>>(h, Hpack,
-                                    W1B1 + (size_t)2048 * 16, W1B2 + (size_t)2048 * 16,
-                                    W2h + (size_t)16 * FF, W2l + (size_t)16 * FF,
-                                    ffb1 + FF, ffb2 + 14, ln2g + 14, ln2b + 14,
-                                    fc1w, fc1b, fc2w, fc2b, x, y,
-                                    B3h, B3l, fc3b, B4h, B4l, fc4b,
-                                    fc5w, fc5b, out, out + NN);
-}
+  layer0_fused<<<256, 512, 0, stream>>>(
+      Qpack0, KB1_0, KB2_0, VhiT0, VloT0, h,
+      wo, bo, ln1g, ln1b,
+      W1B1, W1B2, W2h, W2l, ffb1, ffb2, ln2g, ln2b,
+      wqkv + 42 * 14, bqkv + 42,
+      Qpack1, KB1_1, KB2_1, VhiT1, VloT1);
+
+  layer1_tail<<<256, 512, 0, stream>>>(
+      Qpack1, KB1_1, KB2_1, VhiT1, VloT1, h,
+      wo + 196, bo + 14, ln1g + 14, ln1b + 14,
+      W1B1 + (size_t)2048 * 16, W1B2 + (size_t)2048 * 16,
+      W2h + (size_t)16 * FF, W2l + (size_t)16 * FF,
+      ffb1 + FF, ffb2 + 14, ln2g + 14, ln2b + 14,
+      fc1w, fc1b, fc2w, fc2b, x, y,
+      B3h, B3l, fc3b, B4h, B4l, fc4b,
+      fc5w, fc5b, out, out + NN);
+}
```

Result: faster. 231.1 us (median of 2 runs) (-5.7%).
